# Performance work log

Measured on AMD Instinct MI355X. Metric: run time of the kernel, lower is better.

## Reference

```python
import jax, jax.numpy as jnp
import numpy as np

N = 4096
BATCH = 256
N_IO = 16
EPS = 1.1920929e-07  # torch RMSNorm default eps = finfo(float32).eps


def setup_inputs() -> dict:
    key = jax.random.key(0)
    k_x, k_w = jax.random.split(key)
    x_input = jax.random.normal(k_x, (BATCH, N), dtype=jnp.float32)
    # orthogonal init for W
    a = jax.random.normal(k_w, (N, N), dtype=jnp.float32)
    q, r = jnp.linalg.qr(a)
    W = q * jnp.sign(jnp.diag(r))[None, :]
    B = jnp.zeros((N,), dtype=jnp.float32)
    input_scale = jnp.ones((N_IO,), dtype=jnp.float32)
    output_scale = jnp.ones((N_IO,), dtype=jnp.float32)
    norm_weight = jnp.ones((N,), dtype=jnp.float32)  # RMSNorm elementwise affine
    input_pos = jnp.arange(N_IO, dtype=jnp.int32)            # ids 0..15
    output_pos = jnp.arange(N_IO, dtype=jnp.int32) + (N - N_IO)  # ids 4080..4095
    return {
        "x_input": x_input, "W": W, "B": B,
        "input_scale": input_scale, "output_scale": output_scale,
        "norm_weight": norm_weight,
        "input_pos": input_pos, "output_pos": output_pos,
        "steps": 16,
    }


def reference(x_input, W, B, input_scale, output_scale, norm_weight,
              input_pos, output_pos, steps):
    # dropout is identity in eval mode (rate 0.0)
    def step(h, inj):
        signal = h @ W + B + inj                      # [batch, N]
        a = jnp.tanh(signal)
        ms = jnp.mean(a * a, axis=-1, keepdims=True)
        return a * jax.lax.rsqrt(ms + EPS) * norm_weight

    # pulse mode: scaled input injected only at t == 0
    inj0 = x_input.at[:, input_pos].multiply(input_scale)
    h0 = jnp.zeros_like(x_input)                      # fresh state
    h1 = step(h0, inj0)

    def body(h, _):
        hn = step(h, 0.0)
        return hn, hn

    h_final, rest = jax.lax.scan(body, h1, None, length=steps - 1)  # rest: [steps-1, batch, N]
    outs = jnp.concatenate([h1[:, None, :], jnp.swapaxes(rest, 0, 1)], axis=1)  # [batch, steps, N]
    outs = outs.at[:, :, output_pos].multiply(output_scale)
    return outs, h_final
```

## Files before the change

### kernel.cpp

```cpp
#include <hip/hip_runtime.h>
#include <hip/hip_bf16.h>

#define BATCH 256
#define NDIM  4096
#define STEPS 16
#define EPS_RMS 1.1920929e-07f

typedef _Float16 f16x8 __attribute__((ext_vector_type(8)));
typedef float  f32x4  __attribute__((ext_vector_type(4)));
typedef unsigned short u16x4 __attribute__((ext_vector_type(4)));
typedef unsigned int   u32x4 __attribute__((ext_vector_type(4)));

#define AS1 __attribute__((address_space(1)))
#define AS3 __attribute__((address_space(3)))
#define GLDS16(gp, lp) __builtin_amdgcn_global_load_lds( \
    (const AS1 void*)(gp), (AS3 void*)(lp), 16, 0, 0)
#define SBAR() do { asm volatile("" ::: "memory"); \
                    __builtin_amdgcn_s_barrier();  \
                    asm volatile("" ::: "memory"); } while (0)

__device__ __forceinline__ unsigned short f2h(float f) {
  _Float16 h = (_Float16)f;
  union { _Float16 h; unsigned short u; } v; v.h = h; return v.u;
}

__device__ __forceinline__ float block_reduce_sum_512(float v) {
  __shared__ float ws[8];
  __shared__ float tot;
  #pragma unroll
  for (int off = 32; off > 0; off >>= 1) v += __shfl_down(v, off, 64);
  int lane = threadIdx.x & 63, w = threadIdx.x >> 6;
  if (lane == 0) ws[w] = v;
  __syncthreads();
  if (threadIdx.x == 0) {
    float t = 0.f;
    #pragma unroll
    for (int i = 0; i < 8; ++i) t += ws[i];
    tot = t;
  }
  __syncthreads();
  return tot;
}

__global__ __launch_bounds__(256) void transpose_w(
    const float* __restrict__ W, unsigned short* __restrict__ Wt) {
  __shared__ float tile[64][65];
  int n0 = blockIdx.x * 64;
  int k0 = blockIdx.y * 64;
  int t = threadIdx.x;
  int r = t >> 4, c4 = (t & 15) * 4;
  #pragma unroll
  for (int p = 0; p < 4; ++p) {
    f32x4 v = *(const f32x4*)(W + (size_t)(k0 + r + 16 * p) * NDIM + n0 + c4);
    tile[r + 16 * p][c4 + 0] = v[0];
    tile[r + 16 * p][c4 + 1] = v[1];
    tile[r + 16 * p][c4 + 2] = v[2];
    tile[r + 16 * p][c4 + 3] = v[3];
  }
  __syncthreads();
  #pragma unroll
  for (int p = 0; p < 4; ++p) {
    int nr = r + 16 * p;
    u16x4 o;
    #pragma unroll
    for (int j = 0; j < 4; ++j) o[j] = f2h(tile[c4 + j][nr]);
    *(u16x4*)(Wt + (size_t)(n0 + nr) * NDIM + k0 + c4) = o;
  }
}

__global__ void init_colmul(const float* __restrict__ iscale,
                            const float* __restrict__ oscale,
                            const int* __restrict__ ipos, const int* __restrict__ opos,
                            float* __restrict__ icm, float* __restrict__ ocm) {
  int c = blockIdx.x * 256 + threadIdx.x;
  if (c >= NDIM) return;
  float iv = 1.f, ov = 1.f;
  #pragma unroll
  for (int i = 0; i < 16; ++i) {
    if (ipos[i] == c) iv *= iscale[i];
    if (opos[i] == c) ov *= oscale[i];
  }
  icm[c] = iv; ocm[c] = ov;
}

__global__ __launch_bounds__(512) void step0_kernel(
    const float* __restrict__ x, const float* __restrict__ bias,
    const float* __restrict__ icm, const float* __restrict__ nw,
    const float* __restrict__ ocm,
    unsigned short* __restrict__ hbuf, float* __restrict__ out) {
  int row = blockIdx.x;
  int tid = threadIdx.x;
  const float* xr = x + (size_t)row * NDIM;
  float a[8];
  float sq = 0.f;
  #pragma unroll
  for (int p = 0; p < 2; ++p) {
    int c = p * 2048 + tid * 4;
    f32x4 xv = *(const f32x4*)(xr + c);
    f32x4 bv = *(const f32x4*)(bias + c);
    f32x4 ic = *(const f32x4*)(icm + c);
    #pragma unroll
    for (int j = 0; j < 4; ++j) {
      float av = tanhf(bv[j] + xv[j] * ic[j]);
      a[p * 4 + j] = av;
      sq += av * av;
    }
  }
  float tot = block_reduce_sum_512(sq);
  float scale = rsqrtf(tot * (1.0f / NDIM) + EPS_RMS);
  unsigned short* hrow = hbuf + (size_t)row * NDIM;
  float* orow = out + (size_t)row * STEPS * NDIM;
  #pragma unroll
  for (int p = 0; p < 2; ++p) {
    int c = p * 2048 + tid * 4;
    f32x4 nv = *(const f32x4*)(nw + c);
    f32x4 oc = *(const f32x4*)(ocm + c);
    u16x4 hs; f32x4 os;
    #pragma unroll
    for (int j = 0; j < 4; ++j) {
      float h = a[p * 4 + j] * scale * nv[j];
      hs[j] = f2h(h);
      os[j] = h * oc[j];
    }
    *(u16x4*)(hrow + c) = hs;
    *(f32x4*)(orow + c) = os;
  }
}

__global__ __launch_bounds__(256, 2) void gemm_kernel(
    const unsigned short* __restrict__ A,
    const unsigned short* __restrict__ Bt,
    float* __restrict__ pbuf,
    int kslen) {
  __shared__ __align__(16) unsigned short As[2][128 * 64];
  __shared__ __align__(16) unsigned short Bs[2][128 * 64];
  const int tid = threadIdx.x;
  const int n0 = blockIdx.x * 128;
  const int m0 = blockIdx.y * 128;
  const int ks = blockIdx.z;
  const int kbase = ks * kslen;
  const int nit = kslen >> 6;
  const int wave = tid >> 6, lane = tid & 63;
  const int wm = (wave >> 1) * 64, wn = (wave & 1) * 64;
  const int l15 = lane & 15;
  const int g = lane >> 4;
  const int q = l15 & 7;
  const int srow = tid >> 3;
  const int sch = tid & 7;
  const int koff = (sch ^ (srow & 7)) * 8;

  const unsigned short* aP[4];
  const unsigned short* bP[4];
  #pragma unroll
  for (int i = 0; i < 4; ++i) {
    aP[i] = A + (size_t)(m0 + i * 32 + srow) * NDIM + kbase + koff;
    bP[i] = Bt + (size_t)(n0 + i * 32 + srow) * NDIM + kbase + koff;
  }

  f32x4 acc[4][4];
  f32x4 zero = {0.f, 0.f, 0.f, 0.f};
  #pragma unroll
  for (int i = 0; i < 4; ++i)
    #pragma unroll
    for (int j = 0; j < 4; ++j) acc[i][j] = zero;

  #pragma unroll
  for (int i = 0; i < 4; ++i)
    GLDS16(aP[i], &As[0][(i * 32 + srow) * 64 + sch * 8]);
  #pragma unroll
  for (int i = 0; i < 4; ++i)
    GLDS16(bP[i], &Bs[0][(i * 32 + srow) * 64 + sch * 8]);

  for (int it = 0; it < nit; ++it) {
    const int p = it & 1;
    SBAR();
    if (it < nit - 1) {
      const int kb = (it + 1) * 64;
      #pragma unroll
      for (int i = 0; i < 4; ++i)
        GLDS16(aP[i] + kb, &As[1 - p][(i * 32 + srow) * 64 + sch * 8]);
      #pragma unroll
      for (int i = 0; i < 4; ++i)
        GLDS16(bP[i] + kb, &Bs[1 - p][(i * 32 + srow) * 64 + sch * 8]);
      asm volatile("s_waitcnt vmcnt(8)" ::: "memory");
    } else {
      asm volatile("s_waitcnt vmcnt(0)" ::: "memory");
    }
    SBAR();
    #pragma unroll
    for (int kk = 0; kk < 2; ++kk) {
      f16x8 af[4], bfr[4];
      #pragma unroll
      for (int mf = 0; mf < 4; ++mf) {
        int row = wm + mf * 16 + l15;
        af[mf] = *(const f16x8*)&As[p][row * 64 + (((kk << 2) + g) ^ q) * 8];
      }
      #pragma unroll
      for (int nf = 0; nf < 4; ++nf) {
        int row = wn + nf * 16 + l15;
        bfr[nf] = *(const f16x8*)&Bs[p][row * 64 + (((kk << 2) + g) ^ q) * 8];
      }
      #pragma unroll
      for (int mf = 0; mf < 4; ++mf)
        #pragma unroll
        for (int nf = 0; nf < 4; ++nf)
          acc[mf][nf] = __builtin_amdgcn_mfma_f32_16x16x32_f16(af[mf], bfr[nf], acc[mf][nf], 0, 0, 0);
    }
  }

  float* pout = pbuf + (size_t)ks * BATCH * NDIM;
  const int crow = g * 4;
  #pragma unroll
  for (int mf = 0; mf < 4; ++mf) {
    #pragma unroll
    for (int nf = 0; nf < 4; ++nf) {
      int col = n0 + wn + nf * 16 + l15;
      #pragma unroll
      for (int r = 0; r < 4; ++r) {
        int row = m0 + wm + mf * 16 + crow + r;
        pout[(size_t)row * NDIM + col] = acc[mf][nf][r];
      }
    }
  }
}

__global__ __launch_bounds__(512) void normalize_kernel(
    const float* __restrict__ pbuf, const float* __restrict__ bias,
    const float* __restrict__ nw, const float* __restrict__ ocm,
    unsigned short* __restrict__ hbuf, float* __restrict__ out,
    float* __restrict__ hfin, int t, int is_last, int ksplit) {
  const size_t SL = (size_t)BATCH * NDIM;
  int row = blockIdx.x;
  int tid = threadIdx.x;
  const float* p0 = pbuf + (size_t)row * NDIM;
  float a[8];
  float sq = 0.f;
  #pragma unroll
  for (int p = 0; p < 2; ++p) {
    int c = p * 2048 + tid * 4;
    f32x4 s = *(const f32x4*)(p0 + c);
    for (int k = 1; k < ksplit; ++k)
      s += *(const f32x4*)(p0 + (size_t)k * SL + c);
    f32x4 bv = *(const f32x4*)(bias + c);
    #pragma unroll
    for (int j = 0; j < 4; ++j) {
      float av = tanhf(s[j] + bv[j]);
      a[p * 4 + j] = av;
      sq += av * av;
    }
  }
  float tot = block_reduce_sum_512(sq);
  float scale = rsqrtf(tot * (1.0f / NDIM) + EPS_RMS);
  unsigned short* hrow = hbuf + (size_t)row * NDIM;
  float* orow = out + ((size_t)row * STEPS + t) * NDIM;
  #pragma unroll
  for (int p = 0; p < 2; ++p) {
    int c = p * 2048 + tid * 4;
    f32x4 nv = *(const f32x4*)(nw + c);
    f32x4 oc = *(const f32x4*)(ocm + c);
    u16x4 hs; f32x4 os; f32x4 hv;
    #pragma unroll
    for (int j = 0; j < 4; ++j) {
      float h = a[p * 4 + j] * scale * nv[j];
      hv[j] = h;
      hs[j] = f2h(h);
      os[j] = h * oc[j];
    }
    *(u16x4*)(hrow + c) = hs;
    *(f32x4*)(orow + c) = os;
    if (is_last) *(f32x4*)(hfin + (size_t)row * NDIM + c) = hv;
  }
}

extern "C" void kernel_launch(void* const* d_in, const int* in_sizes, int n_in,
                              void* d_out, int out_size, void* d_ws, size_t ws_size,
                              hipStream_t stream) {
  (void)in_sizes; (void)n_in; (void)out_size;
  const float* x      = (const float*)d_in[0];
  const float* W      = (const float*)d_in[1];
  const float* Bb     = (const float*)d_in[2];
  const float* iscale = (const float*)d_in[3];
  const float* oscale = (const float*)d_in[4];
  const float* nw     = (const float*)d_in[5];
  const int* ipos = (const int*)d_in[6];
  const int* opos = (const int*)d_in[7];

  char* ws = (char*)d_ws;
  unsigned short* Wt   = (unsigned short*)(ws);
  unsigned short* hbuf = (unsigned short*)(ws + 33554432);
  float* icm           = (float*)(ws + 35651584);
  float* ocm           = (float*)(ws + 35667968);
  float* pbuf          = (float*)(ws + 35684352);

  size_t need8 = 35684352 + (size_t)8 * BATCH * NDIM * sizeof(float);
  int ksplit = (ws_size >= need8) ? 8 : 4;
  int kslen = NDIM / ksplit;

  float* out  = (float*)d_out;
  float* hfin = out + (size_t)BATCH * STEPS * NDIM;

  hipLaunchKernelGGL(transpose_w, dim3(64, 64), dim3(256), 0, stream, W, Wt);
  hipLaunchKernelGGL(init_colmul, dim3(16), dim3(256), 0, stream,
                     iscale, oscale, ipos, opos, icm, ocm);
  hipLaunchKernelGGL(step0_kernel, dim3(256), dim3(512), 0, stream,
                     x, Bb, icm, nw, ocm, hbuf, out);
  for (int t = 1; t < STEPS; ++t) {
    hipLaunchKernelGGL(gemm_kernel, dim3(32, 2, ksplit), dim3(256), 0, stream,
                       hbuf, Wt, pbuf, kslen);
    hipLaunchKernelGGL(normalize_kernel, dim3(256), dim3(512), 0, stream,
                       pbuf, Bb, nw, ocm, hbuf, out, hfin, t,
                       (t == STEPS - 1) ? 1 : 0, ksplit);
  }
}
```

Before: 403.6 us.

## Store split-K partials in fp16, halve K tile, raise split-K and occupancy

The GEMM now writes its split-K partial sums as fp16 instead of fp32, which halves partial-buffer traffic. The K tile per iteration shrinks from 64 to 32, cutting LDS use so launch bounds can request 4 blocks per CU. The split-K factor rises from 8 to 16 to put more blocks on the machine, and the normalize kernel is reworked to read 8 contiguous fp16 partials per thread and accumulate them with the bias. Rounding each partial to fp16 adds error and risks overflow, and the normalize kernel now does scalar fp32 stores with a non-contiguous column mapping.

Result: slower. 518.3 us (+28.4%).

```diff
diff --git a/kernel.cpp b/kernel.cpp
--- a/kernel.cpp
+++ b/kernel.cpp
@@ -9,6 +9,7 @@
 typedef _Float16 f16x8 __attribute__((ext_vector_type(8)));
 typedef float  f32x4  __attribute__((ext_vector_type(4)));
 typedef unsigned short u16x4 __attribute__((ext_vector_type(4)));
+typedef unsigned short u16x8 __attribute__((ext_vector_type(8)));
 typedef unsigned int   u32x4 __attribute__((ext_vector_type(4)));
 
 #define AS1 __attribute__((address_space(1)))
@@ -22,6 +23,9 @@
 __device__ __forceinline__ unsigned short f2h(float f) {
   _Float16 h = (_Float16)f;
   union { _Float16 h; unsigned short u; } v; v.h = h; return v.u;
+}
+__device__ __forceinline__ float h2f(unsigned short u) {
+  union { unsigned short u; _Float16 h; } v; v.u = u; return (float)v.h;
 }
 
 __device__ __forceinline__ float block_reduce_sum_512(float v) {
@@ -127,35 +131,32 @@
   }
 }
 
-__global__ __launch_bounds__(256, 2) void gemm_kernel(
+__global__ __launch_bounds__(256, 4) void gemm_kernel(
     const unsigned short* __restrict__ A,
     const unsigned short* __restrict__ Bt,
-    float* __restrict__ pbuf,
+    unsigned short* __restrict__ pbuf,
     int kslen) {
-  __shared__ __align__(16) unsigned short As[2][128 * 64];
-  __shared__ __align__(16) unsigned short Bs[2][128 * 64];
+  __shared__ __align__(16) unsigned short As[2][128 * 32];
+  __shared__ __align__(16) unsigned short Bs[2][128 * 32];
   const int tid = threadIdx.x;
   const int n0 = blockIdx.x * 128;
   const int m0 = blockIdx.y * 128;
   const int ks = blockIdx.z;
   const int kbase = ks * kslen;
-  const int nit = kslen >> 6;
+  const int nit = kslen >> 5;
   const int wave = tid >> 6, lane = tid & 63;
   const int wm = (wave >> 1) * 64, wn = (wave & 1) * 64;
   const int l15 = lane & 15;
   const int g = lane >> 4;
-  const int q = l15 & 7;
-  const int srow = tid >> 3;
-  const int sch = tid & 7;
-  const int koff = (sch ^ (srow & 7)) * 8;
-
-  const unsigned short* aP[4];
-  const unsigned short* bP[4];
-  #pragma unroll
-  for (int i = 0; i < 4; ++i) {
-    aP[i] = A + (size_t)(m0 + i * 32 + srow) * NDIM + kbase + koff;
-    bP[i] = Bt + (size_t)(n0 + i * 32 + srow) * NDIM + kbase + koff;
-  }
+  const int srow = tid >> 2;
+  const int sch = tid & 3;
+  const int ksw = (sch ^ (srow & 3)) * 8;
+
+  const unsigned short* aS0 = A  + (size_t)(m0 + srow) * NDIM + kbase + ksw;
+  const unsigned short* aS1 = aS0 + (size_t)64 * NDIM;
+  const unsigned short* bS0 = Bt + (size_t)(n0 + srow) * NDIM + kbase + ksw;
+  const unsigned short* bS1 = bS0 + (size_t)64 * NDIM;
+  const int ldb = wave * 512;
 
   f32x4 acc[4][4];
   f32x4 zero = {0.f, 0.f, 0.f, 0.f};
@@ -164,51 +165,42 @@
     #pragma unroll
     for (int j = 0; j < 4; ++j) acc[i][j] = zero;
 
-  #pragma unroll
-  for (int i = 0; i < 4; ++i)
-    GLDS16(aP[i], &As[0][(i * 32 + srow) * 64 + sch * 8]);
-  #pragma unroll
-  for (int i = 0; i < 4; ++i)
-    GLDS16(bP[i], &Bs[0][(i * 32 + srow) * 64 + sch * 8]);
+  const int rsw = (g ^ (l15 & 3)) * 8;
+
+  GLDS16(aS0, &As[0][ldb]);
+  GLDS16(aS1, &As[0][2048 + ldb]);
+  GLDS16(bS0, &Bs[0][ldb]);
+  GLDS16(bS1, &Bs[0][2048 + ldb]);
 
   for (int it = 0; it < nit; ++it) {
     const int p = it & 1;
     SBAR();
     if (it < nit - 1) {
-      const int kb = (it + 1) * 64;
-      #pragma unroll
-      for (int i = 0; i < 4; ++i)
-        GLDS16(aP[i] + kb, &As[1 - p][(i * 32 + srow) * 64 + sch * 8]);
-      #pragma unroll
-      for (int i = 0; i < 4; ++i)
-        GLDS16(bP[i] + kb, &Bs[1 - p][(i * 32 + srow) * 64 + sch * 8]);
-      asm volatile("s_waitcnt vmcnt(8)" ::: "memory");
+      const int kb = (it + 1) * 32;
+      GLDS16(aS0 + kb, &As[1 - p][ldb]);
+      GLDS16(aS1 + kb, &As[1 - p][2048 + ldb]);
+      GLDS16(bS0 + kb, &Bs[1 - p][ldb]);
+      GLDS16(bS1 + kb, &Bs[1 - p][2048 + ldb]);
+      asm volatile("s_waitcnt vmcnt(4)" ::: "memory");
     } else {
       asm volatile("s_waitcnt vmcnt(0)" ::: "memory");
     }
     SBAR();
-    #pragma unroll
-    for (int kk = 0; kk < 2; ++kk) {
-      f16x8 af[4], bfr[4];
+    f16x8 af[4], bfr[4];
+    #pragma unroll
+    for (int mf = 0; mf < 4; ++mf)
+      af[mf] = *(const f16x8*)&As[p][(wm + mf * 16 + l15) * 32 + rsw];
+    #pragma unroll
+    for (int nf = 0; nf < 4; ++nf)
+      bfr[nf] = *(const f16x8*)&Bs[p][(wn + nf * 16 + l15) * 32 + rsw];
+    #pragma unroll
+    for (int mf = 0; mf < 4; ++mf)
       #pragma unroll
-      for (int mf = 0; mf < 4; ++mf) {
-        int row = wm + mf * 16 + l15;
-        af[mf] = *(const f16x8*)&As[p][row * 64 + (((kk << 2) + g) ^ q) * 8];
-      }
-      #pragma unroll
-      for (int nf = 0; nf < 4; ++nf) {
-        int row = wn + nf * 16 + l15;
-        bfr[nf] = *(const f16x8*)&Bs[p][row * 64 + (((kk << 2) + g) ^ q) * 8];
-      }
-      #pragma unroll
-      for (int mf = 0; mf < 4; ++mf)
-        #pragma unroll
-        for (int nf = 0; nf < 4; ++nf)
-          acc[mf][nf] = __builtin_amdgcn_mfma_f32_16x16x32_f16(af[mf], bfr[nf], acc[mf][nf], 0, 0, 0);
-    }
-  }
-
-  float* pout = pbuf + (size_t)ks * BATCH * NDIM;
+      for (int nf = 0; nf < 4; ++nf)
+        acc[mf][nf] = __builtin_amdgcn_mfma_f32_16x16x32_f16(af[mf], bfr[nf], acc[mf][nf], 0, 0, 0);
+  }
+
+  unsigned short* pout = pbuf + (size_t)ks * BATCH * NDIM;
   const int crow = g * 4;
   #pragma unroll
   for (int mf = 0; mf < 4; ++mf) {
@@ -218,58 +210,56 @@
       #pragma unroll
       for (int r = 0; r < 4; ++r) {
         int row = m0 + wm + mf * 16 + crow + r;
-        pout[(size_t)row * NDIM + col] = acc[mf][nf][r];
+        pout[(size_t)row * NDIM + col] = f2h(acc[mf][nf][r]);
       }
     }
   }
 }
 
 __global__ __launch_bounds__(512) void normalize_kernel(
-    const float* __restrict__ pbuf, const float* __restrict__ bias,
+    const unsigned short* __restrict__ pbuf, const float* __restrict__ bias,
     const float* __restrict__ nw, const float* __restrict__ ocm,
     unsigned short* __restrict__ hbuf, float* __restrict__ out,
     float* __restrict__ hfin, int t, int is_last, int ksplit) {
   const size_t SL = (size_t)BATCH * NDIM;
   int row = blockIdx.x;
   int tid = threadIdx.x;
-  const float* p0 = pbuf + (size_t)row * NDIM;
+  const unsigned short* p0 = pbuf + (size_t)row * NDIM + tid * 8;
+  float s[8];
+  {
+    const float* b0 = bias + tid * 8;
+    #pragma unroll
+    for (int j = 0; j < 8; ++j) s[j] = b0[j];
+  }
+  for (int k = 0; k < ksplit; ++k) {
+    u16x8 v = *(const u16x8*)(p0 + (size_t)k * SL);
+    #pragma unroll
+    for (int j = 0; j < 8; ++j) s[j] += h2f(v[j]);
+  }
   float a[8];
   float sq = 0.f;
   #pragma unroll
-  for (int p = 0; p < 2; ++p) {
-    int c = p * 2048 + tid * 4;
-    f32x4 s = *(const f32x4*)(p0 + c);
-    for (int k = 1; k < ksplit; ++k)
-      s += *(const f32x4*)(p0 + (size_t)k * SL + c);
-    f32x4 bv = *(const f32x4*)(bias + c);
-    #pragma unroll
-    for (int j = 0; j < 4; ++j) {
-      float av = tanhf(s[j] + bv[j]);
-      a[p * 4 + j] = av;
-      sq += av * av;
-    }
+  for (int j = 0; j < 8; ++j) {
+    float av = tanhf(s[j]);
+    a[j] = av;
+    sq += av * av;
   }
   float tot = block_reduce_sum_512(sq);
   float scale = rsqrtf(tot * (1.0f / NDIM) + EPS_RMS);
-  unsigned short* hrow = hbuf + (size_t)row * NDIM;
-  float* orow = out + ((size_t)row * STEPS + t) * NDIM;
-  #pragma unroll
-  for (int p = 0; p < 2; ++p) {
-    int c = p * 2048 + tid * 4;
-    f32x4 nv = *(const f32x4*)(nw + c);
-    f32x4 oc = *(const f32x4*)(ocm + c);
-    u16x4 hs; f32x4 os; f32x4 hv;
-    #pragma unroll
-    for (int j = 0; j < 4; ++j) {
-      float h = a[p * 4 + j] * scale * nv[j];
-      hv[j] = h;
-      hs[j] = f2h(h);
-      os[j] = h * oc[j];
-    }
-    *(u16x4*)(hrow + c) = hs;
-    *(f32x4*)(orow + c) = os;
-    if (is_last) *(f32x4*)(hfin + (size_t)row * NDIM + c) = hv;
-  }
+  int c = tid * 8;
+  unsigned short* hrow = hbuf + (size_t)row * NDIM + c;
+  float* orow = out + ((size_t)row * STEPS + t) * NDIM + c;
+  const float* nv = nw + c;
+  const float* oc = ocm + c;
+  u16x8 hs;
+  #pragma unroll
+  for (int j = 0; j < 8; ++j) {
+    float h = a[j] * scale * nv[j];
+    hs[j] = f2h(h);
+    orow[j] = h * oc[j];
+    if (is_last) hfin[(size_t)row * NDIM + c + j] = h;
+  }
+  *(u16x8*)hrow = hs;
 }
 
 extern "C" void kernel_launch(void* const* d_in, const int* in_sizes, int n_in,
@@ -290,10 +280,10 @@
   unsigned short* hbuf = (unsigned short*)(ws + 33554432);
   float* icm           = (float*)(ws + 35651584);
   float* ocm           = (float*)(ws + 35667968);
-  float* pbuf          = (float*)(ws + 35684352);
-
-  size_t need8 = 35684352 + (size_t)8 * BATCH * NDIM * sizeof(float);
-  int ksplit = (ws_size >= need8) ? 8 : 4;
+  unsigned short* pbuf = (unsigned short*)(ws + 35684352);
+
+  size_t need16 = 35684352 + (size_t)16 * BATCH * NDIM * sizeof(unsigned short);
+  int ksplit = (ws_size >= need16) ? 16 : 8;
   int kslen = NDIM / ksplit;
 
   float* out  = (float*)d_out;
```

## Store split-K partials in fp16 and move output writes into GEMM epilogue

Applied to the files above, without the earlier changes.

Split-K partial sums are now written and read as fp16 instead of fp32, halving the partial-buffer traffic between the GEMM and normalize kernels. The per-step scaled output is emitted by the next GEMM launch from the fp16 hidden state using ping-pong buffers, so normalize only writes the fp16 state except on the final step. The colmul init is folded into the transpose kernel to save a launch. This trades accuracy: outputs and partials pass through fp16 rounding.

New measurement: 339.1 us. 16.0% less time.

```diff
diff --git a/kernel.cpp b/kernel.cpp
--- a/kernel.cpp
+++ b/kernel.cpp
@@ -9,7 +9,7 @@
 typedef _Float16 f16x8 __attribute__((ext_vector_type(8)));
 typedef float  f32x4  __attribute__((ext_vector_type(4)));
 typedef unsigned short u16x4 __attribute__((ext_vector_type(4)));
-typedef unsigned int   u32x4 __attribute__((ext_vector_type(4)));
+typedef unsigned short u16x8 __attribute__((ext_vector_type(8)));
 
 #define AS1 __attribute__((address_space(1)))
 #define AS3 __attribute__((address_space(3)))
@@ -23,6 +23,9 @@
   _Float16 h = (_Float16)f;
   union { _Float16 h; unsigned short u; } v; v.h = h; return v.u;
 }
+__device__ __forceinline__ float h2f(unsigned short u) {
+  union { unsigned short u; _Float16 h; } v; v.u = u; return (float)v.h;
+}
 
 __device__ __forceinline__ float block_reduce_sum_512(float v) {
   __shared__ float ws[8];
@@ -43,11 +46,24 @@
 }
 
 __global__ __launch_bounds__(256) void transpose_w(
-    const float* __restrict__ W, unsigned short* __restrict__ Wt) {
+    const float* __restrict__ W, unsigned short* __restrict__ Wt,
+    const float* __restrict__ iscale, const float* __restrict__ oscale,
+    const int* __restrict__ ipos, const int* __restrict__ opos,
+    float* __restrict__ icm, float* __restrict__ ocm) {
   __shared__ float tile[64][65];
   int n0 = blockIdx.x * 64;
   int k0 = blockIdx.y * 64;
   int t = threadIdx.x;
+  if (blockIdx.y == 0 && t < 64) {
+    int c = n0 + t;
+    float iv = 1.f, ov = 1.f;
+    #pragma unroll
+    for (int i = 0; i < 16; ++i) {
+      if (ipos[i] == c) iv *= iscale[i];
+      if (opos[i] == c) ov *= oscale[i];
+    }
+    icm[c] = iv; ocm[c] = ov;
+  }
   int r = t >> 4, c4 = (t & 15) * 4;
   #pragma unroll
   for (int p = 0; p < 4; ++p) {
@@ -68,26 +84,10 @@
   }
 }
 
-__global__ void init_colmul(const float* __restrict__ iscale,
-                            const float* __restrict__ oscale,
-                            const int* __restrict__ ipos, const int* __restrict__ opos,
-                            float* __restrict__ icm, float* __restrict__ ocm) {
-  int c = blockIdx.x * 256 + threadIdx.x;
-  if (c >= NDIM) return;
-  float iv = 1.f, ov = 1.f;
-  #pragma unroll
-  for (int i = 0; i < 16; ++i) {
-    if (ipos[i] == c) iv *= iscale[i];
-    if (opos[i] == c) ov *= oscale[i];
-  }
-  icm[c] = iv; ocm[c] = ov;
-}
-
 __global__ __launch_bounds__(512) void step0_kernel(
     const float* __restrict__ x, const float* __restrict__ bias,
     const float* __restrict__ icm, const float* __restrict__ nw,
-    const float* __restrict__ ocm,
-    unsigned short* __restrict__ hbuf, float* __restrict__ out) {
+    unsigned short* __restrict__ hbuf) {
   int row = blockIdx.x;
   int tid = threadIdx.x;
   const float* xr = x + (size_t)row * NDIM;
@@ -109,37 +109,30 @@
   float tot = block_reduce_sum_512(sq);
   float scale = rsqrtf(tot * (1.0f / NDIM) + EPS_RMS);
   unsigned short* hrow = hbuf + (size_t)row * NDIM;
-  float* orow = out + (size_t)row * STEPS * NDIM;
   #pragma unroll
   for (int p = 0; p < 2; ++p) {
     int c = p * 2048 + tid * 4;
     f32x4 nv = *(const f32x4*)(nw + c);
-    f32x4 oc = *(const f32x4*)(ocm + c);
-    u16x4 hs; f32x4 os;
-    #pragma unroll
-    for (int j = 0; j < 4; ++j) {
-      float h = a[p * 4 + j] * scale * nv[j];
-      hs[j] = f2h(h);
-      os[j] = h * oc[j];
-    }
+    u16x4 hs;
+    #pragma unroll
+    for (int j = 0; j < 4; ++j) hs[j] = f2h(a[p * 4 + j] * scale * nv[j]);
     *(u16x4*)(hrow + c) = hs;
-    *(f32x4*)(orow + c) = os;
   }
 }
 
 __global__ __launch_bounds__(256, 2) void gemm_kernel(
     const unsigned short* __restrict__ A,
     const unsigned short* __restrict__ Bt,
-    float* __restrict__ pbuf,
-    int kslen) {
+    unsigned short* __restrict__ pbuf,
+    const float* __restrict__ ocm,
+    float* __restrict__ out, int tm1) {
   __shared__ __align__(16) unsigned short As[2][128 * 64];
   __shared__ __align__(16) unsigned short Bs[2][128 * 64];
   const int tid = threadIdx.x;
   const int n0 = blockIdx.x * 128;
   const int m0 = blockIdx.y * 128;
   const int ks = blockIdx.z;
-  const int kbase = ks * kslen;
-  const int nit = kslen >> 6;
+  const int kbase = ks * 512;
   const int wave = tid >> 6, lane = tid & 63;
   const int wm = (wave >> 1) * 64, wn = (wave & 1) * 64;
   const int l15 = lane & 15;
@@ -171,10 +164,10 @@
   for (int i = 0; i < 4; ++i)
     GLDS16(bP[i], &Bs[0][(i * 32 + srow) * 64 + sch * 8]);
 
-  for (int it = 0; it < nit; ++it) {
+  for (int it = 0; it < 8; ++it) {
     const int p = it & 1;
     SBAR();
-    if (it < nit - 1) {
+    if (it < 7) {
       const int kb = (it + 1) * 64;
       #pragma unroll
       for (int i = 0; i < 4; ++i)
@@ -208,74 +201,99 @@
     }
   }
 
-  float* pout = pbuf + (size_t)ks * BATCH * NDIM;
-  const int crow = g * 4;
-  #pragma unroll
-  for (int mf = 0; mf < 4; ++mf) {
-    #pragma unroll
-    for (int nf = 0; nf < 4; ++nf) {
-      int col = n0 + wn + nf * 16 + l15;
-      #pragma unroll
-      for (int r = 0; r < 4; ++r) {
-        int row = m0 + wm + mf * 16 + crow + r;
-        pout[(size_t)row * NDIM + col] = acc[mf][nf][r];
+  {
+    unsigned short* pout = pbuf + (size_t)ks * BATCH * NDIM;
+    const int crow = g * 4;
+    #pragma unroll
+    for (int mf = 0; mf < 4; ++mf) {
+      #pragma unroll
+      for (int nf = 0; nf < 4; ++nf) {
+        int col = n0 + wn + nf * 16 + l15;
+        #pragma unroll
+        for (int r = 0; r < 4; ++r) {
+          int row = m0 + wm + mf * 16 + crow + r;
+          pout[(size_t)row * NDIM + col] = f2h(acc[mf][nf][r]);
+        }
       }
     }
   }
+
+  {
+    const int col0 = kbase + blockIdx.x * 16;
+    const int row = m0 + (tid >> 1);
+    const int c8 = (tid & 1) * 8;
+    u16x8 hv = *(const u16x8*)(A + (size_t)row * NDIM + col0 + c8);
+    f32x4 oc0 = *(const f32x4*)(ocm + col0 + c8);
+    f32x4 oc1 = *(const f32x4*)(ocm + col0 + c8 + 4);
+    f32x4 o0, o1;
+    #pragma unroll
+    for (int j = 0; j < 4; ++j) {
+      o0[j] = h2f(hv[j]) * oc0[j];
+      o1[j] = h2f(hv[j + 4]) * oc1[j];
+    }
+    float* orow = out + ((size_t)row * STEPS + tm1) * NDIM + col0 + c8;
+    *(f32x4*)orow = o0;
+    *(f32x4*)(orow + 4) = o1;
+  }
 }
 
 __global__ __launch_bounds__(512) void normalize_kernel(
-    const float* __restrict__ pbuf, const float* __restrict__ bias,
+    const unsigned short* __restrict__ pbuf, const float* __restrict__ bias,
     const float* __restrict__ nw, const float* __restrict__ ocm,
     unsigned short* __restrict__ hbuf, float* __restrict__ out,
-    float* __restrict__ hfin, int t, int is_last, int ksplit) {
+    float* __restrict__ hfin, int is_last) {
   const size_t SL = (size_t)BATCH * NDIM;
   int row = blockIdx.x;
   int tid = threadIdx.x;
-  const float* p0 = pbuf + (size_t)row * NDIM;
+  int c = tid * 8;
+  const unsigned short* p0 = pbuf + (size_t)row * NDIM + c;
+  float s[8];
+  {
+    const float* b0 = bias + c;
+    #pragma unroll
+    for (int j = 0; j < 8; ++j) s[j] = b0[j];
+  }
+  #pragma unroll
+  for (int k = 0; k < 8; ++k) {
+    u16x8 v = *(const u16x8*)(p0 + (size_t)k * SL);
+    #pragma unroll
+    for (int j = 0; j < 8; ++j) s[j] += h2f(v[j]);
+  }
   float a[8];
   float sq = 0.f;
   #pragma unroll
-  for (int p = 0; p < 2; ++p) {
-    int c = p * 2048 + tid * 4;
-    f32x4 s = *(const f32x4*)(p0 + c);
-    for (int k = 1; k < ksplit; ++k)
-      s += *(const f32x4*)(p0 + (size_t)k * SL + c);
-    f32x4 bv = *(const f32x4*)(bias + c);
-    #pragma unroll
-    for (int j = 0; j < 4; ++j) {
-      float av = tanhf(s[j] + bv[j]);
-      a[p * 4 + j] = av;
-      sq += av * av;
-    }
+  for (int j = 0; j < 8; ++j) {
+    float av = tanhf(s[j]);
+    a[j] = av;
+    sq += av * av;
   }
   float tot = block_reduce_sum_512(sq);
   float scale = rsqrtf(tot * (1.0f / NDIM) + EPS_RMS);
-  unsigned short* hrow = hbuf + (size_t)row * NDIM;
-  float* orow = out + ((size_t)row * STEPS + t) * NDIM;
-  #pragma unroll
-  for (int p = 0; p < 2; ++p) {
-    int c = p * 2048 + tid * 4;
-    f32x4 nv = *(const f32x4*)(nw + c);
-    f32x4 oc = *(const f32x4*)(ocm + c);
-    u16x4 hs; f32x4 os; f32x4 hv;
-    #pragma unroll
-    for (int j = 0; j < 4; ++j) {
-      float h = a[p * 4 + j] * scale * nv[j];
-      hv[j] = h;
+  unsigned short* hrow = hbuf + (size_t)row * NDIM + c;
+  const float* nv = nw + c;
+  u16x8 hs;
+  if (is_last) {
+    float* orow = out + ((size_t)row * STEPS + (STEPS - 1)) * NDIM + c;
+    float* frow = hfin + (size_t)row * NDIM + c;
+    const float* oc = ocm + c;
+    #pragma unroll
+    for (int j = 0; j < 8; ++j) {
+      float h = a[j] * scale * nv[j];
       hs[j] = f2h(h);
-      os[j] = h * oc[j];
-    }
-    *(u16x4*)(hrow + c) = hs;
-    *(f32x4*)(orow + c) = os;
-    if (is_last) *(f32x4*)(hfin + (size_t)row * NDIM + c) = hv;
-  }
+      orow[j] = h * oc[j];
+      frow[j] = h;
+    }
+  } else {
+    #pragma unroll
+    for (int j = 0; j < 8; ++j) hs[j] = f2h(a[j] * scale * nv[j]);
+  }
+  *(u16x8*)hrow = hs;
 }
 
 extern "C" void kernel_launch(void* const* d_in, const int* in_sizes, int n_in,
                               void* d_out, int out_size, void* d_ws, size_t ws_size,
                               hipStream_t stream) {
-  (void)in_sizes; (void)n_in; (void)out_size;
+  (void)in_sizes; (void)n_in; (void)out_size; (void)ws_size;
   const float* x      = (const float*)d_in[0];
   const float* W      = (const float*)d_in[1];
   const float* Bb     = (const float*)d_in[2];
@@ -287,28 +305,25 @@
 
   char* ws = (char*)d_ws;
   unsigned short* Wt   = (unsigned short*)(ws);
-  unsigned short* hbuf = (unsigned short*)(ws + 33554432);
-  float* icm           = (float*)(ws + 35651584);
-  float* ocm           = (float*)(ws + 35667968);
-  float* pbuf          = (float*)(ws + 35684352);
-
-  size_t need8 = 35684352 + (size_t)8 * BATCH * NDIM * sizeof(float);
-  int ksplit = (ws_size >= need8) ? 8 : 4;
-  int kslen = NDIM / ksplit;
+  unsigned short* hA   = (unsigned short*)(ws + 33554432);
+  unsigned short* hB   = (unsigned short*)(ws + 35651584);
+  float* icm           = (float*)(ws + 37748736);
+  float* ocm           = (float*)(ws + 37765120);
+  unsigned short* pbuf = (unsigned short*)(ws + 37781504);
 
   float* out  = (float*)d_out;
   float* hfin = out + (size_t)BATCH * STEPS * NDIM;
 
-  hipLaunchKernelGGL(transpose_w, dim3(64, 64), dim3(256), 0, stream, W, Wt);
-  hipLaunchKernelGGL(init_colmul, dim3(16), dim3(256), 0, stream,
-                     iscale, oscale, ipos, opos, icm, ocm);
+  hipLaunchKernelGGL(transpose_w, dim3(64, 64), dim3(256), 0, stream,
+                     W, Wt, iscale, oscale, ipos, opos, icm, ocm);
   hipLaunchKernelGGL(step0_kernel, dim3(256), dim3(512), 0, stream,
-                     x, Bb, icm, nw, ocm, hbuf, out);
+                     x, Bb, icm, nw, hA);
   for (int t = 1; t < STEPS; ++t) {
-    hipLaunchKernelGGL(gemm_kernel, dim3(32, 2, ksplit), dim3(256), 0, stream,
-                       hbuf, Wt, pbuf, kslen);
+    const unsigned short* Ap = ((t - 1) & 1) ? hB : hA;
+    unsigned short* Ac = (t & 1) ? hB : hA;
+    hipLaunchKernelGGL(gemm_kernel, dim3(32, 2, 8), dim3(256), 0, stream,
+                       Ap, Wt, pbuf, ocm, out, t - 1);
     hipLaunchKernelGGL(normalize_kernel, dim3(256), dim3(512), 0, stream,
-                       pbuf, Bb, nw, ocm, hbuf, out, hfin, t,
-                       (t == STEPS - 1) ? 1 : 0, ksplit);
-  }
-}
+                       pbuf, Bb, nw, ocm, Ac, out, hfin, (t == STEPS - 1) ? 1 : 0);
+  }
+}
```
